# Performance work log

Measured on AMD Instinct MI355X. Metric: run time of the kernel, lower is better.

The kernel has to match this reference:

```python
import jax, jax.numpy as jnp
import numpy as np

RMIN, RMAX, MAX_PHASE = 0.9, 1.0, 6.283


def setup_inputs() -> dict:
    key = jax.random.key(0)
    ks = jax.random.split(key, 12)
    Bsz, T, U, O, S, H = 16, 4096, 128, 128, 256, 512
    inp = jax.random.normal(ks[0], (Bsz, T, U), dtype=jnp.float32)
    # stable complex diagonal: |lambda| in [RMIN, RMAX], phase in [0, MAX_PHASE]
    r = RMIN + (RMAX - RMIN) * jax.random.uniform(ks[1], (S,), dtype=jnp.float32)
    theta = MAX_PHASE * jax.random.uniform(ks[2], (S,), dtype=jnp.float32)
    Lambda_re = r * jnp.cos(theta)
    Lambda_im = r * jnp.sin(theta)
    B = jax.random.normal(ks[3], (S, U), dtype=jnp.float32) / np.sqrt(U)
    C = jax.random.normal(ks[4], (O, S), dtype=jnp.float32) / np.sqrt(S)
    D = jax.random.normal(ks[5], (O, U), dtype=jnp.float32) / np.sqrt(U)
    W1 = jax.random.normal(ks[6], (H, O), dtype=jnp.float32) / np.sqrt(O)
    W2 = jax.random.normal(ks[7], (H, H), dtype=jnp.float32) / np.sqrt(H)
    W3 = jax.random.normal(ks[8], (O, H), dtype=jnp.float32) / np.sqrt(H)
    Wlin = jax.random.normal(ks[9], (O, U), dtype=jnp.float32) / np.sqrt(U)
    return {"input": inp, "Lambda_re": Lambda_re, "Lambda_im": Lambda_im,
            "B": B, "C": C, "D": D, "W1": W1, "W2": W2, "W3": W3, "Wlin": Wlin}


def _linear_scan(lam, bu):
    # lam: (S,) complex; bu: (B, T, S) complex
    # h_t = lam * h_{t-1} + bu_t, h_0 = 0  (work-efficient associative scan)
    A = jnp.broadcast_to(lam[None, None, :], bu.shape)

    def combine(c1, c2):
        a1, x1 = c1
        a2, x2 = c2
        return a1 * a2, a2 * x1 + x2

    _, h = jax.lax.associative_scan(combine, (A, bu), axis=1)
    return h


def reference(input, Lambda_re, Lambda_im, B, C, D, W1, W2, W3, Wlin):
    lam = (Lambda_re + 1j * Lambda_im).astype(jnp.complex64)        # (S,)
    bu = jnp.einsum('btu,su->bts', input, B).astype(jnp.complex64)   # (B,T,S)
    h = _linear_scan(lam, bu)                                        # (B,T,S) complex
    # LRU readout: real(C h) + D u
    y = jnp.einsum('bts,os->bto', h, C.astype(jnp.complex64)).real \
        + jnp.einsum('btu,ou->bto', input, D)                        # (B,T,O)
    # MLP: Linear->SiLU->Linear->ReLU->Linear (no biases)
    z = jax.nn.silu(y @ W1.T)
    z = jax.nn.relu(z @ W2.T)
    mlp_out = z @ W3.T                                               # (B,T,O)
    # residual linear path
    return mlp_out + input @ Wlin.T
```

## Files before the change

kernel.cpp:

```cpp
#include <hip/hip_runtime.h>
#include <hip/hip_bf16.h>

#define BSZ 16
#define TT 4096
#define UU 128
#define OO 128
#define SS 256
#define HH 512
#define BT (BSZ*TT)
#define CLEN 64
#define NCH (TT/CLEN)

using bf16x8 = __attribute__((ext_vector_type(8))) short;
using f32x4  = __attribute__((ext_vector_type(4))) float;

__device__ __forceinline__ unsigned short f2bf(float x){
  union { float f; unsigned int u; } v; v.f = x;
  unsigned int r = v.u + 0x7fffu + ((v.u >> 16) & 1u);
  return (unsigned short)(r >> 16);
}
__device__ __forceinline__ float bf2f(unsigned short h){
  union { float f; unsigned int u; } v; v.u = ((unsigned int)h) << 16;
  return v.f;
}

#define GLD16(g, s) __builtin_amdgcn_global_load_lds( \
    (const __attribute__((address_space(1))) unsigned int*)(g), \
    (__attribute__((address_space(3))) unsigned int*)(s), 16, 0, 0)

#define SBAR() do{ __builtin_amdgcn_sched_barrier(0); \
                   __builtin_amdgcn_s_barrier(); \
                   __builtin_amdgcn_sched_barrier(0); }while(0)

__global__ __launch_bounds__(256) void split_k(const float* __restrict__ x,
                                               unsigned short* __restrict__ H,
                                               unsigned short* __restrict__ L, int n4){
  int i = blockIdx.x * 256 + threadIdx.x;
  if (i >= n4) return;
  float4 v = ((const float4*)x)[i];
  unsigned short h0 = f2bf(v.x), h1 = f2bf(v.y), h2 = f2bf(v.z), h3 = f2bf(v.w);
  ushort4 hh = make_ushort4(h0, h1, h2, h3);
  ushort4 ll = make_ushort4(f2bf(v.x - bf2f(h0)), f2bf(v.y - bf2f(h1)),
                            f2bf(v.z - bf2f(h2)), f2bf(v.w - bf2f(h3)));
  ((ushort4*)H)[i] = hh;
  ((ushort4*)L)[i] = ll;
}

struct WJobs {
  const float* src[7];
  unsigned short* H[7];
  unsigned short* L[7];
  int end4[7];
};
__global__ __launch_bounds__(256) void split_w(WJobs j, int total4){
  int i = blockIdx.x * 256 + threadIdx.x;
  if (i >= total4) return;
  int t = 0, base = 0;
  #pragma unroll
  for (int k = 0; k < 7; k++){
    if (i >= j.end4[k]){ t = k + 1; base = j.end4[k]; }
  }
  int idx = i - base;
  float4 v = ((const float4*)j.src[t])[idx];
  unsigned short h0 = f2bf(v.x), h1 = f2bf(v.y), h2 = f2bf(v.z), h3 = f2bf(v.w);
  ushort4 hh = make_ushort4(h0, h1, h2, h3);
  ushort4 ll = make_ushort4(f2bf(v.x - bf2f(h0)), f2bf(v.y - bf2f(h1)),
                            f2bf(v.z - bf2f(h2)), f2bf(v.w - bf2f(h3)));
  ((ushort4*)j.H[t])[idx] = hh;
  ((ushort4*)j.L[t])[idx] = ll;
}

__global__ __launch_bounds__(256, 2) void gemm_split(
    const unsigned short* __restrict__ AH1, const unsigned short* __restrict__ AL1,
    const unsigned short* __restrict__ BH1, const unsigned short* __restrict__ BL1, int K1, int f1,
    const unsigned short* __restrict__ AH2, const unsigned short* __restrict__ AL2,
    const unsigned short* __restrict__ BH2, const unsigned short* __restrict__ BL2, int K2, int f2,
    unsigned short* __restrict__ outH, unsigned short* __restrict__ outL,
    float* __restrict__ outF, int Nout, int EPI,
    const float* __restrict__ lre, const float* __restrict__ lim,
    float2* __restrict__ ends)
{
  __shared__ __align__(16) unsigned short SM[32768];
  unsigned short* Ah = SM;
  unsigned short* Al = SM + 8192;
  unsigned short* Bh = SM + 16384;
  unsigned short* Bl = SM + 24576;

  const int tid = threadIdx.x;
  const int mb = blockIdx.x, nb = blockIdx.y;
  const int l = tid & 63, w = tid >> 6;
  const int wr = w >> 1, wc = w & 1;
  const int fr = l & 15, fq = l >> 4;

  f32x4 acc[4][4];
  #pragma unroll
  for (int m = 0; m < 4; m++)
    #pragma unroll
    for (int n = 0; n < 4; n++) acc[m][n] = f32x4{0.f, 0.f, 0.f, 0.f};

  const int nkt = (K1 + K2) >> 5;

  auto STAGE = [&](int buf, int kt){
    const int k0 = kt << 5;
    const unsigned short *aH, *aL, *bH, *bL; int st, kk, flg;
    if (k0 < K1){ aH = AH1; aL = AL1; bH = BH1; bL = BL1; st = K1; kk = k0; flg = f1; }
    else        { aH = AH2; aL = AL2; bH = BH2; bL = BL2; st = K2; kk = k0 - K1; flg = f2; }
    #pragma unroll
    for (int it = 0; it < 2; it++){
      int seg = tid + it * 256;
      int r = seg >> 2, c4 = seg & 3;
      int sc = (c4 ^ ((r >> 1) & 3)) << 3;
      size_t go = (size_t)(mb*128 + r) * st + kk + sc;
      size_t gb = (size_t)(nb*128 + r) * st + kk + sc;
      int lo = buf*4096 + r*32 + c4*8;
      GLD16(aH + go, Ah + lo);
      if (flg & 1) GLD16(aL + go, Al + lo);
      GLD16(bH + gb, Bh + lo);
      if (flg & 2) GLD16(bL + gb, Bl + lo);
    }
  };

  STAGE(0, 0);
  __syncthreads();

  for (int kt = 0; kt < nkt; kt++){
    const int cur = kt & 1;
    const int flg = ((kt << 5) < K1) ? f1 : f2;
    if (kt + 1 < nkt) STAGE(cur ^ 1, kt + 1);

    bf16x8 a_h[4], a_l[4], b_h[4], b_l[4];
    #pragma unroll
    for (int m = 0; m < 4; m++){
      int lra = wr*64 + m*16 + fr;
      int ra = cur*4096 + lra*32 + ((fq ^ ((lra >> 1) & 3)) << 3);
      a_h[m] = *(const bf16x8*)&Ah[ra];
      if (flg & 1) a_l[m] = *(const bf16x8*)&Al[ra];
      int lrb = wc*64 + m*16 + fr;
      int rb = cur*4096 + lrb*32 + ((fq ^ ((lrb >> 1) & 3)) << 3);
      b_h[m] = *(const bf16x8*)&Bh[rb];
      if (flg & 2) b_l[m] = *(const bf16x8*)&Bl[rb];
    }
    __builtin_amdgcn_s_setprio(1);
    #pragma unroll
    for (int m = 0; m < 4; m++)
      #pragma unroll
      for (int n = 0; n < 4; n++)
        acc[m][n] = __builtin_amdgcn_mfma_f32_16x16x32_bf16(a_h[m], b_h[n], acc[m][n], 0, 0, 0);
    if (flg & 1)
      #pragma unroll
      for (int m = 0; m < 4; m++)
        #pragma unroll
        for (int n = 0; n < 4; n++)
          acc[m][n] = __builtin_amdgcn_mfma_f32_16x16x32_bf16(a_l[m], b_h[n], acc[m][n], 0, 0, 0);
    if (flg & 2)
      #pragma unroll
      for (int m = 0; m < 4; m++)
        #pragma unroll
        for (int n = 0; n < 4; n++)
          acc[m][n] = __builtin_amdgcn_mfma_f32_16x16x32_bf16(a_h[m], b_l[n], acc[m][n], 0, 0, 0);
    __builtin_amdgcn_s_setprio(0);

    __syncthreads();
  }

  float* fl = (float*)SM;
  #pragma unroll
  for (int m = 0; m < 4; m++)
    #pragma unroll
    for (int n = 0; n < 4; n++)
      #pragma unroll
      for (int j = 0; j < 4; j++)
        fl[(wr*64 + m*16 + fq*4 + j)*128 + wc*64 + n*16 + fr] = acc[m][n][j];
  __syncthreads();
  #pragma unroll
  for (int it = 0; it < 8; it++){
    int task = tid + (it << 8);
    int rl = task >> 4, cg = task & 15;
    float4 v0 = *(const float4*)&fl[rl*128 + cg*8];
    float4 v1 = *(const float4*)&fl[rl*128 + cg*8 + 4];
    size_t o = (size_t)(mb*128 + rl) * Nout + nb*128 + cg*8;
    if (EPI == 0){
      *(float4*)(outF + o)     = v0;
      *(float4*)(outF + o + 4) = v1;
    } else {
      float xv[8] = {v0.x,v0.y,v0.z,v0.w,v1.x,v1.y,v1.z,v1.w};
      union { unsigned short us[8]; uint4 v; } ph, pl;
      #pragma unroll
      for (int e = 0; e < 8; e++){
        float x = xv[e];
        if (EPI == 2)      x = x / (1.f + __expf(-x));
        else if (EPI == 3) x = fmaxf(x, 0.f);
        ph.us[e] = f2bf(x);
        pl.us[e] = f2bf(x - bf2f(ph.us[e]));
      }
      *(uint4*)(outH + o) = ph.v;
      if (outL) *(uint4*)(outL + o) = pl.v;
    }
  }
  if (ends){
    int c = tid >> 7, sl = tid & 127;
    int b = mb >> 5, chunk = ((mb & 31) << 1) + c;
    int s = nb*128 + sl;
    float lr = lre[s], li = lim[s];
    float hr = 0.f, hi2 = 0.f;
    for (int t = 0; t < 64; t++){
      float x = fl[(c*64 + t)*128 + sl];
      float nr = fmaf(lr, hr, fmaf(-li, hi2, x));
      float ni = fmaf(lr, hi2, li * hr);
      hr = nr; hi2 = ni;
    }
    ends[((size_t)(b*NCH + chunk))*SS + s] = make_float2(hr, hi2);
  }
}

#define S0OFF 65536
#define S1OFF 98304
#define S2OFF 131072

__global__ __launch_bounds__(512, 1) void mlp_fused(
    const unsigned short* __restrict__ yH,
    const unsigned short* __restrict__ W1H,
    const unsigned short* __restrict__ W2H,
    unsigned short* __restrict__ z2H)
{
  __shared__ __align__(16) unsigned char LDS[163840];
  const int tid = threadIdx.x;
  const int l = tid & 63, w = tid >> 6;
  const int fr = l & 15, fq = l >> 4;
  const size_t r0 = (size_t)blockIdx.x * 64;

  auto stageW2 = [&](int kt, int slotoff){
    #pragma unroll
    for (int it = 0; it < 4; it++){
      int seg = tid + (it << 9);
      int r = seg >> 2, c4 = seg & 3;
      GLD16(W2H + (size_t)r * HH + kt*32 + ((c4 ^ ((r >> 1) & 3)) << 3),
            LDS + slotoff + seg*16);
    }
  };

  #pragma unroll
  for (int it = 0; it < 16; it++){
    int seg = tid + (it << 9);
    int r = seg >> 4, c16 = seg & 15;
    GLD16(W1H + (size_t)r * UU + ((c16 ^ (r & 7)) << 3), LDS + seg*16);
  }
  #pragma unroll
  for (int it = 0; it < 2; it++){
    int seg = tid + (it << 9);
    int r = seg >> 4, c16 = seg & 15;
    GLD16(yH + (size_t)(r0 + r) * UU + ((c16 ^ (r & 7)) << 3),
          LDS + S2OFF + seg*16);
  }
  asm volatile("s_waitcnt vmcnt(0)" ::: "memory");
  SBAR();

  f32x4 acc[4][4];
  #pragma unroll
  for (int m = 0; m < 4; m++)
    #pragma unroll
    for (int n = 0; n < 4; n++) acc[m][n] = f32x4{0.f, 0.f, 0.f, 0.f};

  #pragma unroll
  for (int kt = 0; kt < 4; kt++){
    bf16x8 a[4], b[4];
    #pragma unroll
    for (int m = 0; m < 4; m++){
      int row = m*16 + fr, kc = kt*4 + fq;
      a[m] = *(const bf16x8*)(LDS + S2OFF + (row*128 + ((kc ^ (row & 7)) << 3))*2);
    }
    #pragma unroll
    for (int n = 0; n < 4; n++){
      int lrb = w*64 + n*16 + fr, kc = kt*4 + fq;
      b[n] = *(const bf16x8*)(LDS + (lrb*128 + ((kc ^ (lrb & 7)) << 3))*2);
    }
    __builtin_amdgcn_s_setprio(1);
    #pragma unroll
    for (int m = 0; m < 4; m++)
      #pragma unroll
      for (int n = 0; n < 4; n++)
        acc[m][n] = __builtin_amdgcn_mfma_f32_16x16x32_bf16(a[m], b[n], acc[m][n], 0, 0, 0);
    __builtin_amdgcn_s_setprio(0);
  }
  SBAR();

  stageW2(0, S0OFF);
  stageW2(1, S1OFF);

  unsigned short* Z1 = (unsigned short*)LDS;
  #pragma unroll
  for (int m = 0; m < 4; m++)
    #pragma unroll
    for (int n = 0; n < 4; n++)
      #pragma unroll
      for (int j = 0; j < 4; j++){
        float x = acc[m][n][j];
        x = x / (1.f + __expf(-x));
        int row = m*16 + fq*4 + j;
        int col = w*64 + n*16 + fr;
        int c64 = col >> 3, ce = col & 7;
        Z1[row*512 + ((c64 ^ (row & 7)) << 3) + ce] = f2bf(x);
      }
  SBAR();

  #pragma unroll
  for (int m = 0; m < 4; m++)
    #pragma unroll
    for (int n = 0; n < 4; n++) acc[m][n] = f32x4{0.f, 0.f, 0.f, 0.f};

  for (int kt = 0; kt < 16; kt++){
    if (kt < 15) asm volatile("s_waitcnt vmcnt(4)" ::: "memory");
    else         asm volatile("s_waitcnt vmcnt(0)" ::: "memory");
    SBAR();
    if (kt + 2 < 16){
      int so = (kt + 2) % 3;
      stageW2(kt + 2, so == 0 ? S0OFF : (so == 1 ? S1OFF : S2OFF));
    }
    const int cs = kt % 3;
    const unsigned char* Wb = LDS + (cs == 0 ? S0OFF : (cs == 1 ? S1OFF : S2OFF));
    bf16x8 a[4], b[4];
    #pragma unroll
    for (int m = 0; m < 4; m++){
      int row = m*16 + fr, kc = kt*4 + fq;
      a[m] = *(const bf16x8*)(LDS + (row*512 + ((kc ^ (row & 7)) << 3))*2);
    }
    #pragma unroll
    for (int n = 0; n < 4; n++){
      int lrb = w*64 + n*16 + fr;
      b[n] = *(const bf16x8*)(Wb + (lrb*32 + ((fq ^ ((lrb >> 1) & 3)) << 3))*2);
    }
    __builtin_amdgcn_s_setprio(1);
    #pragma unroll
    for (int m = 0; m < 4; m++)
      #pragma unroll
      for (int n = 0; n < 4; n++)
        acc[m][n] = __builtin_amdgcn_mfma_f32_16x16x32_bf16(a[m], b[n], acc[m][n], 0, 0, 0);
    __builtin_amdgcn_s_setprio(0);
  }
  SBAR();

  unsigned short* EP = (unsigned short*)(LDS + S0OFF);
  #pragma unroll
  for (int m = 0; m < 4; m++)
    #pragma unroll
    for (int n = 0; n < 4; n++)
      #pragma unroll
      for (int j = 0; j < 4; j++){
        float x = fmaxf(acc[m][n][j], 0.f);
        EP[(m*16 + fq*4 + j)*512 + w*64 + n*16 + fr] = f2bf(x);
      }
  __syncthreads();
  #pragma unroll
  for (int it = 0; it < 8; it++){
    int seg = tid + (it << 9);
    int r = seg >> 6, c8 = seg & 63;
    *(uint4*)(z2H + (r0 + r)*HH + c8*8) = *(const uint4*)&EP[r*512 + c8*8];
  }
}

__global__ __launch_bounds__(256) void scan_carries(const float2* __restrict__ ends,
                                                    const float* __restrict__ lre,
                                                    const float* __restrict__ lim,
                                                    float2* __restrict__ carryin){
  const int idx = blockIdx.x * 256 + threadIdx.x;
  const int b = idx >> 8;
  const int s = idx & 255;
  float pr = lre[s], pi = lim[s];
  #pragma unroll
  for (int q = 0; q < 6; q++){
    float nr = pr*pr - pi*pi;
    float ni = 2.f * pr * pi;
    pr = nr; pi = ni;
  }
  float hr = 0.f, hi = 0.f;
  for (int c = 0; c < NCH; c++){
    size_t o = ((size_t)b*NCH + c)*SS + s;
    carryin[o] = make_float2(hr, hi);
    float2 e = ends[o];
    float nr = fmaf(pr, hr, fmaf(-pi, hi, e.x));
    float ni = fmaf(pr, hi, fmaf(pi, hr, e.y));
    hr = nr; hi = ni;
  }
}

__global__ __launch_bounds__(256) void scan_apply_v(
    const unsigned short* __restrict__ buH, const unsigned short* __restrict__ buL,
    const float* __restrict__ lre, const float* __restrict__ lim,
    const float2* __restrict__ carryin, unsigned short* __restrict__ RehH){
  const int tid = threadIdx.x;
  const int grp = tid >> 6, ln = tid & 63;
  const int chunk = blockIdx.x * 4 + grp;
  const int b = chunk >> 6, ch = chunk & 63;
  const int s0 = ln * 4;
  float lr[4], li[4], hr[4], hi[4];
  #pragma unroll
  for (int e = 0; e < 4; e++){ lr[e] = lre[s0+e]; li[e] = lim[s0+e]; }
  const float2* ci = &carryin[((size_t)(b*NCH + ch))*SS + s0];
  #pragma unroll
  for (int e = 0; e < 4; e++){ hr[e] = ci[e].x; hi[e] = ci[e].y; }
  const size_t rbase = ((size_t)b*TT + (size_t)ch*CLEN)*SS + s0;
  for (int t = 0; t < CLEN; t++){
    uint2 hv = *(const uint2*)(buH + rbase + (size_t)t*SS);
    uint2 lv = *(const uint2*)(buL + rbase + (size_t)t*SS);
    const unsigned short* hs = (const unsigned short*)&hv;
    const unsigned short* ls = (const unsigned short*)&lv;
    uint2 ov; unsigned short* os = (unsigned short*)&ov;
    #pragma unroll
    for (int e = 0; e < 4; e++){
      float x = bf2f(hs[e]) + bf2f(ls[e]);
      float nr = fmaf(lr[e], hr[e], fmaf(-li[e], hi[e], x));
      float ni = fmaf(lr[e], hi[e], li[e] * hr[e]);
      hr[e] = nr; hi[e] = ni;
      os[e] = f2bf(nr);
    }
    *(uint2*)(RehH + rbase + (size_t)t*SS) = ov;
  }
}

extern "C" void kernel_launch(void* const* d_in, const int* in_sizes, int n_in,
                              void* d_out, int out_size, void* d_ws, size_t ws_size,
                              hipStream_t stream){
  const float* inp = (const float*)d_in[0];
  const float* lre = (const float*)d_in[1];
  const float* lim = (const float*)d_in[2];
  const float* Bm  = (const float*)d_in[3];
  const float* Cm  = (const float*)d_in[4];
  const float* Dm  = (const float*)d_in[5];
  const float* W1  = (const float*)d_in[6];
  const float* W2  = (const float*)d_in[7];
  const float* W3  = (const float*)d_in[8];
  const float* Wl  = (const float*)d_in[9];
  float* out = (float*)d_out;

  char* ws = (char*)d_ws;
  size_t off = 0;
  auto alloc = [&](size_t bytes)->char*{
    char* p = ws + off; off += (bytes + 255) & ~(size_t)255; return p;
  };
  unsigned short* inH  = (unsigned short*)alloc((size_t)BT*UU*2);
  unsigned short* inL  = (unsigned short*)alloc((size_t)BT*UU*2);
  char* Rbu = alloc((size_t)BT*SS*2*2);
  unsigned short* buH = (unsigned short*)Rbu;
  unsigned short* buL = (unsigned short*)(Rbu + (size_t)BT*SS*2);
  char* R2 = alloc((size_t)BT*HH*2);
  unsigned short* RehH = (unsigned short*)R2;
  unsigned short* yH   = (unsigned short*)(R2 + (size_t)BT*SS*2);
  unsigned short* z2H  = (unsigned short*)Rbu;
  unsigned short* BwH = (unsigned short*)alloc((size_t)SS*UU*2);
  unsigned short* BwL = (unsigned short*)alloc((size_t)SS*UU*2);
  unsigned short* CH_ = (unsigned short*)alloc((size_t)OO*SS*2);
  unsigned short* CL_ = (unsigned short*)alloc((size_t)OO*SS*2);
  unsigned short* DH_ = (unsigned short*)alloc((size_t)OO*UU*2);
  unsigned short* DL_ = (unsigned short*)alloc((size_t)OO*UU*2);
  unsigned short* W1H = (unsigned short*)alloc((size_t)HH*OO*2);
  unsigned short* W1L = (unsigned short*)alloc((size_t)HH*OO*2);
  unsigned short* W2H = (unsigned short*)alloc((size_t)HH*HH*2);
  unsigned short* W2L = (unsigned short*)alloc((size_t)HH*HH*2);
  unsigned short* W3H = (unsigned short*)alloc((size_t)OO*HH*2);
  unsigned short* W3L = (unsigned short*)alloc((size_t)OO*HH*2);
  unsigned short* WlH = (unsigned short*)alloc((size_t)OO*UU*2);
  unsigned short* WlL = (unsigned short*)alloc((size_t)OO*UU*2);
  float2* ends    = (float2*)alloc((size_t)BSZ*NCH*SS*8);
  float2* carryin = (float2*)alloc((size_t)BSZ*NCH*SS*8);
  if (off > ws_size) return;

  split_k<<<(BT*UU/4 + 255)/256, 256, 0, stream>>>(inp, inH, inL, BT*UU/4);
  {
    WJobs j;
    const float* srcs[7] = {Bm, Cm, Dm, W1, W2, W3, Wl};
    unsigned short* Hs[7] = {BwH, CH_, DH_, W1H, W2H, W3H, WlH};
    unsigned short* Ls[7] = {BwL, CL_, DL_, W1L, W2L, W3L, WlL};
    int n4s[7] = {SS*UU/4, OO*SS/4, OO*UU/4, HH*OO/4, HH*HH/4, OO*HH/4, OO*UU/4};
    int cum = 0;
    for (int k = 0; k < 7; k++){
      j.src[k] = srcs[k]; j.H[k] = Hs[k]; j.L[k] = Ls[k];
      cum += n4s[k]; j.end4[k] = cum;
    }
    split_w<<<(cum + 255)/256, 256, 0, stream>>>(j, cum);
  }

  gemm_split<<<dim3(BT/128, SS/128), 256, 0, stream>>>(
      inH, inL, BwH, BwL, UU, 3,
      inH, inL, BwH, BwL, 0,  3,
      buH, buL, nullptr, SS, 1,
      lre, lim, ends);

  scan_carries<<<(BSZ*SS)/256, 256, 0, stream>>>(ends, lre, lim, carryin);

  scan_apply_v<<<BSZ*NCH/4, 256, 0, stream>>>(buH, buL, lre, lim, carryin, RehH);

  gemm_split<<<dim3(BT/128, OO/128), 256, 0, stream>>>(
      RehH, RehH, CH_, CL_, SS, 2,
      inH,  inL,  DH_, DL_, UU, 3,
      yH, nullptr, nullptr, OO, 1,
      nullptr, nullptr, nullptr);

  mlp_fused<<<BT/64, 512, 0, stream>>>(yH, W1H, W2H, z2H);

  gemm_split<<<dim3(BT/128, OO/128), 256, 0, stream>>>(
      z2H, z2H, W3H, W3L, HH, 2,
      inH, inL, WlH, WlL, UU, 3,
      nullptr, nullptr, out, OO, 0,
      nullptr, nullptr, nullptr);
}
```

Measured before the change: 211.6 us.

## Stage W2 per-wave into private LDS slices to drop per-iteration block barriers

Each wave now loads only the 64 W2 rows it consumes into its own LDS slice with a triple-buffered rotation. This removes the block-wide barrier inside the 16-step K loop, since each wave only waits on its own vmcnt. The Z1 intermediate is stored in a k-chunk-major layout so A-fragment reads become contiguous without the XOR swizzle, which may add LDS bank conflicts on the writes. The W2 prefetch is issued after the MFMAs instead of before them, and slot reuse now depends on per-wave ordering being correct.

```diff
diff --git a/kernel.cpp b/kernel.cpp
--- a/kernel.cpp
+++ b/kernel.cpp
@@ -213,9 +213,8 @@
   }
 }
 
-#define S0OFF 65536
-#define S1OFF 98304
-#define S2OFF 131072
+#define WS_OFF 65536
+#define YOFF   131072
 
 __global__ __launch_bounds__(512, 1) void mlp_fused(
     const unsigned short* __restrict__ yH,
@@ -229,14 +228,20 @@
   const int fr = l & 15, fq = l >> 4;
   const size_t r0 = (size_t)blockIdx.x * 64;
 
-  auto stageW2 = [&](int kt, int slotoff){
-    #pragma unroll
-    for (int it = 0; it < 4; it++){
-      int seg = tid + (it << 9);
-      int r = seg >> 2, c4 = seg & 3;
-      GLD16(W2H + (size_t)r * HH + kt*32 + ((c4 ^ ((r >> 1) & 3)) << 3),
-            LDS + slotoff + seg*16);
-    }
+  const unsigned short* w2base[4];
+  int w2lds[4];
+  #pragma unroll
+  for (int it = 0; it < 4; it++){
+    int seg = l + (it << 6);
+    int r = seg >> 2, c4 = seg & 3;
+    w2base[it] = W2H + (size_t)(w*64 + r) * HH + ((c4 ^ ((r >> 1) & 3)) << 3);
+    w2lds[it] = WS_OFF + w*12288 + seg*16;
+  }
+  auto stageW2 = [&](int kt){
+    const int so = (kt % 3) * 4096;
+    #pragma unroll
+    for (int it = 0; it < 4; it++)
+      GLD16(w2base[it] + kt*32, LDS + w2lds[it] + so);
   };
 
   #pragma unroll
@@ -250,7 +255,7 @@
     int seg = tid + (it << 9);
     int r = seg >> 4, c16 = seg & 15;
     GLD16(yH + (size_t)(r0 + r) * UU + ((c16 ^ (r & 7)) << 3),
-          LDS + S2OFF + seg*16);
+          LDS + YOFF + seg*16);
   }
   asm volatile("s_waitcnt vmcnt(0)" ::: "memory");
   SBAR();
@@ -267,7 +272,7 @@
     #pragma unroll
     for (int m = 0; m < 4; m++){
       int row = m*16 + fr, kc = kt*4 + fq;
-      a[m] = *(const bf16x8*)(LDS + S2OFF + (row*128 + ((kc ^ (row & 7)) << 3))*2);
+      a[m] = *(const bf16x8*)(LDS + YOFF + (row*128 + ((kc ^ (row & 7)) << 3))*2);
     }
     #pragma unroll
     for (int n = 0; n < 4; n++){
@@ -284,8 +289,8 @@
   }
   SBAR();
 
-  stageW2(0, S0OFF);
-  stageW2(1, S1OFF);
+  stageW2(0);
+  stageW2(1);
 
   unsigned short* Z1 = (unsigned short*)LDS;
   #pragma unroll
@@ -298,8 +303,7 @@
         x = x / (1.f + __expf(-x));
         int row = m*16 + fq*4 + j;
         int col = w*64 + n*16 + fr;
-        int c64 = col >> 3, ce = col & 7;
-        Z1[row*512 + ((c64 ^ (row & 7)) << 3) + ce] = f2bf(x);
+        Z1[(col >> 3)*512 + row*8 + (col & 7)] = f2bf(x);
       }
   SBAR();
 
@@ -311,23 +315,16 @@
   for (int kt = 0; kt < 16; kt++){
     if (kt < 15) asm volatile("s_waitcnt vmcnt(4)" ::: "memory");
     else         asm volatile("s_waitcnt vmcnt(0)" ::: "memory");
-    SBAR();
-    if (kt + 2 < 16){
-      int so = (kt + 2) % 3;
-      stageW2(kt + 2, so == 0 ? S0OFF : (so == 1 ? S1OFF : S2OFF));
-    }
-    const int cs = kt % 3;
-    const unsigned char* Wb = LDS + (cs == 0 ? S0OFF : (cs == 1 ? S1OFF : S2OFF));
+    __builtin_amdgcn_sched_barrier(0);
+    const unsigned char* Wb = LDS + WS_OFF + w*12288 + (kt % 3)*4096;
     bf16x8 a[4], b[4];
     #pragma unroll
-    for (int m = 0; m < 4; m++){
-      int row = m*16 + fr, kc = kt*4 + fq;
-      a[m] = *(const bf16x8*)(LDS + (row*512 + ((kc ^ (row & 7)) << 3))*2);
-    }
+    for (int m = 0; m < 4; m++)
+      a[m] = *(const bf16x8*)(LDS + (size_t)(kt*4 + fq)*1024 + (m*16 + fr)*16);
     #pragma unroll
     for (int n = 0; n < 4; n++){
-      int lrb = w*64 + n*16 + fr;
-      b[n] = *(const bf16x8*)(Wb + (lrb*32 + ((fq ^ ((lrb >> 1) & 3)) << 3))*2);
+      int rl = n*16 + fr;
+      b[n] = *(const bf16x8*)(Wb + rl*64 + ((fq ^ ((rl >> 1) & 3)) << 4));
     }
     __builtin_amdgcn_s_setprio(1);
     #pragma unroll
@@ -336,10 +333,11 @@
       for (int n = 0; n < 4; n++)
         acc[m][n] = __builtin_amdgcn_mfma_f32_16x16x32_bf16(a[m], b[n], acc[m][n], 0, 0, 0);
     __builtin_amdgcn_s_setprio(0);
+    if (kt + 2 < 16) stageW2(kt + 2);
   }
   SBAR();
 
-  unsigned short* EP = (unsigned short*)(LDS + S0OFF);
+  unsigned short* EP = (unsigned short*)(LDS + WS_OFF);
   #pragma unroll
   for (int m = 0; m < 4; m++)
     #pragma unroll
```

New measurement: 207.6 us. About the same (-1.9%).
